# Kernel tuning notes

Measured on AMD Instinct MI355X. Metric: run time of the kernel, lower is better.

## Reference

```python
import jax, jax.numpy as jnp
import numpy as np

B, T, C, H = 4, 2048, 1024, 16


def setup_inputs() -> dict:
    key = jax.random.key(0)
    k1, k2, k3 = jax.random.split(key, 3)
    x = jax.random.normal(k1, (B, T, C), dtype=jnp.float32)
    Wqkv = jax.random.normal(k2, (C, 3 * C), dtype=jnp.float32) * 0.02
    bqkv = jnp.zeros((3 * C,), dtype=jnp.float32)
    Wproj = jax.random.normal(k3, (C, C), dtype=jnp.float32) * 0.02
    bproj = jnp.zeros((C,), dtype=jnp.float32)
    return {"x": x, "Wqkv": Wqkv, "bqkv": bqkv, "Wproj": Wproj, "bproj": bproj}


def reference(x, Wqkv, bqkv, Wproj, bproj):
    Bx, Tx, Cx = x.shape
    head = Cx // H
    qkv = x @ Wqkv + bqkv                      # [B,T,3C]
    q, k, v = jnp.split(qkv, 3, axis=-1)
    q = q.reshape(Bx, Tx, H, head)
    k = k.reshape(Bx, Tx, H, head)
    v = v.reshape(Bx, Tx, H, head)
    scale = 1.0 / jnp.sqrt(jnp.asarray(head, dtype=x.dtype))
    scores = jnp.einsum('bqhd,bkhd->bhqk', q, k) * scale   # [B,H,T,T]
    causal = jnp.tril(jnp.ones((Tx, Tx), dtype=bool))       # [T,T]
    neg = jnp.finfo(x.dtype).min
    scores = jnp.where(causal[None, None, :, :], scores, neg)
    probs = jax.nn.softmax(scores, axis=-1)
    y = jnp.einsum('bhqk,bkhd->bqhd', probs, v).reshape(Bx, Tx, Cx)
    return y @ Wproj + bproj
```

## Files before the change

### kernel.cpp

```cpp
#include <hip/hip_runtime.h>
#include <stdint.h>

#define BB 4
#define TT 2048
#define CC 1024
#define HH 16

typedef __bf16 bf16x8 __attribute__((ext_vector_type(8)));
typedef float f32x4 __attribute__((ext_vector_type(4)));
typedef float f32x16 __attribute__((ext_vector_type(16)));
typedef unsigned short ushort8 __attribute__((ext_vector_type(8)));
typedef unsigned short ushort4v __attribute__((ext_vector_type(4)));

__device__ __forceinline__ unsigned short f2b(float f) {
    union { float f; unsigned u; } v; v.f = f;
    unsigned r = v.u + 0x7FFFu + ((v.u >> 16) & 1u);
    return (unsigned short)(r >> 16);
}
__device__ __forceinline__ unsigned pack2(float a, float b) {
    union { float f; unsigned u; } ua, ub; ua.f = a; ub.f = b;
    return __builtin_amdgcn_perm(ub.u + 0x8000u, ua.u + 0x8000u, 0x07060302u);
}
__device__ __forceinline__ float fexp2(float x) {
#if __has_builtin(__builtin_amdgcn_exp2f)
    return __builtin_amdgcn_exp2f(x);
#else
    return exp2f(x);
#endif
}
#define LOG2E 1.4426950408889634f

#define ASYNC16(gp, lp) __builtin_amdgcn_global_load_lds( \
    (const __attribute__((address_space(1))) void*)(gp),  \
    (__attribute__((address_space(3))) void*)(lp), 16, 0, 0)

__global__ __launch_bounds__(256) void k_prep(const float* __restrict__ x,
                                              const float* __restrict__ Wqkv,
                                              const float* __restrict__ Wproj,
                                              unsigned short* __restrict__ x16,
                                              unsigned short* __restrict__ wqkvT,
                                              unsigned short* __restrict__ wprojT) {
    __shared__ float tile[32][33];
    const int bid = blockIdx.x;
    const int t = threadIdx.x;
    if (bid < 8192) {
        int i = (bid * 256 + t) * 4;
        float4 v = *(const float4*)(x + i);
        ushort4v o;
        o.x = f2b(v.x); o.y = f2b(v.y); o.z = f2b(v.z); o.w = f2b(v.w);
        *(ushort4v*)(x16 + i) = o;
        return;
    }
    const float* in; unsigned short* out; int R, Cc, bx, by;
    if (bid < 11264) {
        int b2 = bid - 8192;
        in = Wqkv; out = wqkvT; R = 1024; Cc = 3072;
        bx = (b2 % 96) * 32; by = (b2 / 96) * 32;
    } else {
        int b3 = bid - 11264;
        in = Wproj; out = wprojT; R = 1024; Cc = 1024;
        bx = (b3 & 31) * 32; by = (b3 >> 5) * 32;
    }
    int tx = t & 31, ty = t >> 5;
    for (int i = 0; i < 32; i += 8)
        tile[ty + i][tx] = in[(size_t)(by + ty + i) * Cc + bx + tx];
    __syncthreads();
    for (int i = 0; i < 32; i += 8)
        out[(size_t)(bx + ty + i) * R + by + tx] = f2b(tile[tx][ty + i]);
}

#define QSCALE 0.125f
template <int MODE>
__global__ __launch_bounds__(256) void k_gemm(const unsigned short* __restrict__ A,
                                              const unsigned short* __restrict__ Bt,
                                              const float* __restrict__ bias,
                                              float* __restrict__ outf,
                                              unsigned short* __restrict__ qo,
                                              unsigned short* __restrict__ ko,
                                              unsigned short* __restrict__ vo,
                                              int M, int N, int K) {
    __shared__ unsigned short sm[8704];
    unsigned short* As = sm;
    unsigned short* Bs = sm + 4096;
    const int t = threadIdx.x;
    const int lane = t & 63;
    const int c = lane & 15, qd = lane >> 4;
    const int wave = t >> 6;
    const int wr = (wave >> 1) * 64, wc = (wave & 1) * 64;
    const int bm = blockIdx.x * 128, bn = blockIdx.y * 128;

    f32x4 acc[4][4] = {};

    const unsigned short* Ap = A + (size_t)(bm + (t >> 2)) * K + (t & 3) * 8;
    const unsigned short* Bp = Bt + (size_t)(bn + (t >> 2)) * K + (t & 3) * 8;
    unsigned short* Asw = &As[t * 8];
    unsigned short* Bsw = &Bs[t * 8];

    for (int k0 = 0; k0 < K; k0 += 32) {
        __syncthreads();
        ASYNC16(Ap + k0, Asw);
        ASYNC16(Ap + (size_t)64 * K + k0, Asw + 2048);
        ASYNC16(Bp + k0, Bsw);
        ASYNC16(Bp + (size_t)64 * K + k0, Bsw + 2048);
        __syncthreads();
        bf16x8 af[4], bfr[4];
        for (int i = 0; i < 4; i++)
            af[i] = *(const bf16x8*)&As[(wr + i * 16 + c) * 32 + qd * 8];
        for (int j = 0; j < 4; j++)
            bfr[j] = *(const bf16x8*)&Bs[(wc + j * 16 + c) * 32 + qd * 8];
        for (int i = 0; i < 4; i++)
            for (int j = 0; j < 4; j++)
                acc[i][j] = __builtin_amdgcn_mfma_f32_16x16x32_bf16(af[i], bfr[j], acc[i][j], 0, 0, 0);
    }

    for (int j = 0; j < 4; j++) {
        float bv = bias[bn + wc + j * 16 + c];
        for (int i = 0; i < 4; i++)
            for (int r = 0; r < 4; r++)
                acc[i][j][r] += bv;
    }

    if (MODE == 0) {
        float* smf = (float*)sm;
        for (int p = 0; p < 4; p++) {
            __syncthreads();
            int lr0 = (wr >> 2) + qd * 4;
            for (int j = 0; j < 4; j++) {
                int col = wc + j * 16 + c;
                for (int r = 0; r < 4; r++)
                    smf[(lr0 + r) * 132 + col] = acc[p][j][r];
            }
            __syncthreads();
            for (int op = 0; op < 4; op++) {
                int lr = (t >> 5) + op * 8;
                int ch = (t & 31) * 4;
                float4 v = *(float4*)&smf[lr * 132 + ch];
                int grow = bm + (lr >> 4) * 64 + 16 * p + (lr & 15);
                *(float4*)&outf[(size_t)grow * N + bn + ch] = v;
            }
        }
    } else if (bn < 2048) {
        unsigned short* dst = (bn < 1024) ? qo : ko;
        const int dcol0 = (bn < 1024) ? bn : bn - 1024;
        const float sc = (bn < 1024) ? QSCALE : 1.0f;
        for (int p = 0; p < 2; p++) {
            __syncthreads();
            for (int ii = 0; ii < 2; ii++) {
                int i = 2 * p + ii;
                int lr0 = (wr >> 1) + ii * 16 + qd * 4;
                for (int j = 0; j < 4; j++) {
                    int col = wc + j * 16 + c;
                    for (int r = 0; r < 4; r++)
                        sm[(lr0 + r) * 136 + col] = f2b(acc[i][j][r] * sc);
                }
            }
            __syncthreads();
            for (int op = 0; op < 4; op++) {
                int lr = (t >> 4) + op * 16;
                int ch = (t & 15) * 8;
                ushort8 v = *(ushort8*)&sm[lr * 136 + ch];
                int grow = bm + (lr >> 5) * 64 + 32 * p + (lr & 31);
                *(ushort8*)&dst[(size_t)grow * 1024 + dcol0 + ch] = v;
            }
        }
    } else {
        const int bseg = bm >> 11;
        const int bmt = bm & 2047;
        for (int p = 0; p < 2; p++) {
            __syncthreads();
            for (int jj = 0; jj < 2; jj++) {
                int j = 2 * p + jj;
                int dl = (wc >> 1) + jj * 16 + c;
                for (int i = 0; i < 4; i++) {
                    int tl = wr + i * 16 + qd * 4;
                    ushort4v pk;
                    pk.x = f2b(acc[i][j][0]); pk.y = f2b(acc[i][j][1]);
                    pk.z = f2b(acc[i][j][2]); pk.w = f2b(acc[i][j][3]);
                    *(ushort4v*)&sm[dl * 136 + tl] = pk;
                }
            }
            __syncthreads();
            for (int op = 0; op < 4; op++) {
                int dl = (t >> 4) + op * 16;
                int ch = (t & 15) * 8;
                ushort8 v = *(ushort8*)&sm[dl * 136 + ch];
                int d = (bn - 2048) + (dl >> 5) * 64 + 32 * p + (dl & 31);
                *(ushort8*)&vo[((size_t)bseg * 1024 + d) * 2048 + bmt + ch] = v;
            }
        }
    }
}

__global__ __launch_bounds__(256, 4) void k_attn(const unsigned short* __restrict__ q16,
                                                 const unsigned short* __restrict__ k16,
                                                 const unsigned short* __restrict__ vT16,
                                                 unsigned short* __restrict__ y16) {
    const int h = blockIdx.y, b = blockIdx.z;
    const int qi = (((int)blockIdx.x + h) & 15) ^ ((b & 1) ? 15 : 0);
    __shared__ unsigned short smem[2 * 9216];
    unsigned short* q_s = smem;
    const int t = threadIdx.x, lane = t & 63, wave = t >> 6;
    const int l31 = lane & 31, hl = lane >> 5;
    const int wq = wave * 32;

    {
        int row = t >> 1, c32 = (t & 1) * 32;
        const unsigned short* src = q16 + ((size_t)(b * TT + qi * 128 + row)) * CC + h * 64 + c32;
        ushort8 v0 = *(const ushort8*)(src);
        ushort8 v1 = *(const ushort8*)(src + 8);
        ushort8 v2 = *(const ushort8*)(src + 16);
        ushort8 v3 = *(const ushort8*)(src + 24);
        *(ushort8*)&q_s[row * 72 + c32] = v0;
        *(ushort8*)&q_s[row * 72 + c32 + 8] = v1;
        *(ushort8*)&q_s[row * 72 + c32 + 16] = v2;
        *(ushort8*)&q_s[row * 72 + c32 + 24] = v3;
    }
    __syncthreads();
    bf16x8 qf[4];
    for (int s = 0; s < 4; s++)
        qf[s] = *(const bf16x8*)&q_s[(wq + l31) * 72 + s * 16 + hl * 8];
    __syncthreads();

    f32x16 oacc[2] = {};
    float m = -3e38f, l = 0.f;
    const int qmaxw = qi * 128 + wq + 31;
    const int qminw = qi * 128 + wq;
    const int qg = qi * 128 + wq + l31;
    const int jn = 2 * qi + 2;
    const unsigned short* kbase = k16 + (size_t)b * TT * CC + h * 64;
    const unsigned short* vbase = vT16 + (((size_t)b * 16 + h) * 64) * TT;

    const int row = t >> 2, c16 = (t & 3) * 16;
    const unsigned short* ksrc = kbase + (size_t)row * CC + c16;
    const unsigned short* vsrc = vbase + (size_t)row * TT + c16;
    ushort8 ka = *(const ushort8*)ksrc, kb = *(const ushort8*)(ksrc + 8);
    ushort8 va = *(const ushort8*)vsrc, vb = *(const ushort8*)(vsrc + 8);

    for (int j = 0; j < jn; j++) {
        unsigned short* k_s = smem + (j & 1) * 9216;
        unsigned short* vt_s = k_s + 4608;
        *(ushort8*)&k_s[row * 72 + c16] = ka;
        *(ushort8*)&k_s[row * 72 + c16 + 8] = kb;
        *(ushort8*)&vt_s[row * 72 + c16] = va;
        *(ushort8*)&vt_s[row * 72 + c16 + 8] = vb;
        __syncthreads();
        if (j + 1 < jn) {
            const unsigned short* kn = ksrc + (size_t)(j + 1) * 64 * CC;
            const unsigned short* vn = vsrc + (j + 1) * 64;
            ka = *(const ushort8*)kn; kb = *(const ushort8*)(kn + 8);
            va = *(const ushort8*)vn; vb = *(const ushort8*)(vn + 8);
        }
        if (j * 64 > qmaxw) continue;

        f32x16 sacc[2] = {};
        for (int c2 = 0; c2 < 2; c2++)
            for (int s = 0; s < 4; s++) {
                bf16x8 kf = *(const bf16x8*)&k_s[(c2 * 32 + l31) * 72 + s * 16 + hl * 8];
                sacc[c2] = __builtin_amdgcn_mfma_f32_32x32x16_bf16(kf, qf[s], sacc[c2], 0, 0, 0);
            }

        if (j * 64 + 63 > qminw) {
            for (int c2 = 0; c2 < 2; c2++)
                for (int r = 0; r < 16; r++) {
                    int kvg = j * 64 + c2 * 32 + (r & 3) + 8 * (r >> 2) + 4 * hl;
                    if (kvg > qg) sacc[c2][r] = -1e30f;
                }
        }

        float mx = -1e30f;
        for (int c2 = 0; c2 < 2; c2++)
            for (int r = 0; r < 16; r++) mx = fmaxf(mx, sacc[c2][r]);
        mx = fmaxf(mx, __shfl_xor(mx, 32, 64));
        float mn = fmaxf(m, mx);
        float negmnl = -mn * LOG2E;
        float alpha = fexp2(fmaf(m, LOG2E, negmnl));
        m = mn;
        float sum = 0.f;
        unsigned pg[2][4][2];
        for (int c2 = 0; c2 < 2; c2++)
            for (int g = 0; g < 4; g++) {
                float p0 = fexp2(fmaf(sacc[c2][g * 4 + 0], LOG2E, negmnl));
                float p1 = fexp2(fmaf(sacc[c2][g * 4 + 1], LOG2E, negmnl));
                float p2 = fexp2(fmaf(sacc[c2][g * 4 + 2], LOG2E, negmnl));
                float p3 = fexp2(fmaf(sacc[c2][g * 4 + 3], LOG2E, negmnl));
                sum += (p0 + p1) + (p2 + p3);
                pg[c2][g][0] = pack2(p0, p1);
                pg[c2][g][1] = pack2(p2, p3);
            }
        sum += __shfl_xor(sum, 32, 64);
        l = l * alpha + sum;
        if (__ballot(alpha != 1.0f)) {
            for (int c2 = 0; c2 < 2; c2++)
                for (int r = 0; r < 16; r++) oacc[c2][r] *= alpha;
        }

        bf16x8 pf[4];
        for (int c2 = 0; c2 < 2; c2++)
            for (int pr = 0; pr < 2; pr++) {
                unsigned se0 = hl ? pg[c2][2 * pr][0] : pg[c2][2 * pr + 1][0];
                unsigned se1 = hl ? pg[c2][2 * pr][1] : pg[c2][2 * pr + 1][1];
                unsigned r0 = (unsigned)__shfl_xor((int)se0, 32, 64);
                unsigned r1 = (unsigned)__shfl_xor((int)se1, 32, 64);
                union { unsigned u[4]; bf16x8 v; } fr;
                fr.u[0] = hl ? r0 : pg[c2][2 * pr][0];
                fr.u[1] = hl ? r1 : pg[c2][2 * pr][1];
                fr.u[2] = hl ? pg[c2][2 * pr + 1][0] : r0;
                fr.u[3] = hl ? pg[c2][2 * pr + 1][1] : r1;
                pf[c2 * 2 + pr] = fr.v;
            }

        for (int s = 0; s < 4; s++)
            for (int c2o = 0; c2o < 2; c2o++) {
                bf16x8 vf = *(const bf16x8*)&vt_s[(c2o * 32 + l31) * 72 + s * 16 + hl * 8];
                oacc[c2o] = __builtin_amdgcn_mfma_f32_32x32x16_bf16(vf, pf[s], oacc[c2o], 0, 0, 0);
            }
    }

    float rl = 1.0f / l;
    size_t rowb = ((size_t)b * TT + qg) * CC + h * 64;
    for (int c2 = 0; c2 < 2; c2++)
        for (int g = 0; g < 4; g++) {
            ushort4v pk;
            pk.x = f2b(oacc[c2][g * 4 + 0] * rl);
            pk.y = f2b(oacc[c2][g * 4 + 1] * rl);
            pk.z = f2b(oacc[c2][g * 4 + 2] * rl);
            pk.w = f2b(oacc[c2][g * 4 + 3] * rl);
            *(ushort4v*)&y16[rowb + c2 * 32 + g * 8 + hl * 4] = pk;
        }
}

extern "C" void kernel_launch(void* const* d_in, const int* in_sizes, int n_in,
                              void* d_out, int out_size, void* d_ws, size_t ws_size,
                              hipStream_t stream) {
    const float* x     = (const float*)d_in[0];
    const float* Wqkv  = (const float*)d_in[1];
    const float* bqkv  = (const float*)d_in[2];
    const float* Wproj = (const float*)d_in[3];
    const float* bproj = (const float*)d_in[4];
    float* out = (float*)d_out;

    const int M = BB * TT;
    unsigned short* x16    = (unsigned short*)d_ws;
    unsigned short* y16    = x16;
    unsigned short* wqkvT  = x16 + (size_t)M * CC;
    unsigned short* wprojT = wqkvT + (size_t)3 * CC * CC;
    unsigned short* q16    = wprojT + (size_t)CC * CC;
    unsigned short* k16    = q16 + (size_t)M * CC;
    unsigned short* vT16   = k16 + (size_t)M * CC;

    k_prep<<<12288, 256, 0, stream>>>(x, Wqkv, Wproj, x16, wqkvT, wprojT);
    k_gemm<1><<<dim3(M / 128, 3 * CC / 128), 256, 0, stream>>>(x16, wqkvT, bqkv, nullptr,
                                                               q16, k16, vT16, M, 3 * CC, CC);
    k_attn<<<dim3(TT / 128, HH, BB), 256, 0, stream>>>(q16, k16, vT16, y16);
    k_gemm<0><<<dim3(M / 128, CC / 128), 256, 0, stream>>>(y16, wprojT, bproj, out,
                                                           nullptr, nullptr, nullptr, M, CC, CC);
}
```

Before: 263.7 us.

## Deepen GEMM K-step to 64 and single-buffer attention K/V shared memory

The GEMM main loop now loads two 32-wide K slices per iteration into separate LDS halves, so each iteration does two MFMA passes and half as many barrier pairs run. The attention kernel drops its double-buffered K/V shared memory and reuses one 128x72 buffer, with a barrier at the top of each iteration in place of the one after the Q load. The GEMM change doubles its LDS footprint, and the attention change shrinks LDS to raise occupancy but may serialize the LDS store against the previous iteration's reads.

```diff
diff --git a/kernel.cpp b/kernel.cpp
--- a/kernel.cpp
+++ b/kernel.cpp
@@ -79,9 +79,11 @@
                                               unsigned short* __restrict__ ko,
                                               unsigned short* __restrict__ vo,
                                               int M, int N, int K) {
-    __shared__ unsigned short sm[8704];
-    unsigned short* As = sm;
-    unsigned short* Bs = sm + 4096;
+    __shared__ unsigned short sm[16384];
+    unsigned short* AsLo = sm;
+    unsigned short* AsHi = sm + 4096;
+    unsigned short* BsLo = sm + 8192;
+    unsigned short* BsHi = sm + 12288;
     const int t = threadIdx.x;
     const int lane = t & 63;
     const int c = lane & 15, qd = lane >> 4;
@@ -93,24 +95,30 @@
 
     const unsigned short* Ap = A + (size_t)(bm + (t >> 2)) * K + (t & 3) * 8;
     const unsigned short* Bp = Bt + (size_t)(bn + (t >> 2)) * K + (t & 3) * 8;
-    unsigned short* Asw = &As[t * 8];
-    unsigned short* Bsw = &Bs[t * 8];
-
-    for (int k0 = 0; k0 < K; k0 += 32) {
+
+    for (int k0 = 0; k0 < K; k0 += 64) {
         __syncthreads();
-        ASYNC16(Ap + k0, Asw);
-        ASYNC16(Ap + (size_t)64 * K + k0, Asw + 2048);
-        ASYNC16(Bp + k0, Bsw);
-        ASYNC16(Bp + (size_t)64 * K + k0, Bsw + 2048);
+        ASYNC16(Ap + k0, &AsLo[t * 8]);
+        ASYNC16(Ap + (size_t)64 * K + k0, &AsLo[t * 8 + 2048]);
+        ASYNC16(Ap + k0 + 32, &AsHi[t * 8]);
+        ASYNC16(Ap + (size_t)64 * K + k0 + 32, &AsHi[t * 8 + 2048]);
+        ASYNC16(Bp + k0, &BsLo[t * 8]);
+        ASYNC16(Bp + (size_t)64 * K + k0, &BsLo[t * 8 + 2048]);
+        ASYNC16(Bp + k0 + 32, &BsHi[t * 8]);
+        ASYNC16(Bp + (size_t)64 * K + k0 + 32, &BsHi[t * 8 + 2048]);
         __syncthreads();
-        bf16x8 af[4], bfr[4];
-        for (int i = 0; i < 4; i++)
-            af[i] = *(const bf16x8*)&As[(wr + i * 16 + c) * 32 + qd * 8];
-        for (int j = 0; j < 4; j++)
-            bfr[j] = *(const bf16x8*)&Bs[(wc + j * 16 + c) * 32 + qd * 8];
-        for (int i = 0; i < 4; i++)
+        for (int s = 0; s < 2; s++) {
+            const unsigned short* Asp = s ? AsHi : AsLo;
+            const unsigned short* Bsp = s ? BsHi : BsLo;
+            bf16x8 af[4], bfr[4];
+            for (int i = 0; i < 4; i++)
+                af[i] = *(const bf16x8*)&Asp[(wr + i * 16 + c) * 32 + qd * 8];
             for (int j = 0; j < 4; j++)
-                acc[i][j] = __builtin_amdgcn_mfma_f32_16x16x32_bf16(af[i], bfr[j], acc[i][j], 0, 0, 0);
+                bfr[j] = *(const bf16x8*)&Bsp[(wc + j * 16 + c) * 32 + qd * 8];
+            for (int i = 0; i < 4; i++)
+                for (int j = 0; j < 4; j++)
+                    acc[i][j] = __builtin_amdgcn_mfma_f32_16x16x32_bf16(af[i], bfr[j], acc[i][j], 0, 0, 0);
+        }
     }
 
     for (int j = 0; j < 4; j++) {
@@ -197,8 +205,10 @@
                                                  unsigned short* __restrict__ y16) {
     const int h = blockIdx.y, b = blockIdx.z;
     const int qi = (((int)blockIdx.x + h) & 15) ^ ((b & 1) ? 15 : 0);
-    __shared__ unsigned short smem[2 * 9216];
+    __shared__ unsigned short smem[128 * 72];
     unsigned short* q_s = smem;
+    unsigned short* k_s = smem;
+    unsigned short* vt_s = smem + 64 * 72;
     const int t = threadIdx.x, lane = t & 63, wave = t >> 6;
     const int l31 = lane & 31, hl = lane >> 5;
     const int wq = wave * 32;
@@ -219,7 +229,6 @@
     bf16x8 qf[4];
     for (int s = 0; s < 4; s++)
         qf[s] = *(const bf16x8*)&q_s[(wq + l31) * 72 + s * 16 + hl * 8];
-    __syncthreads();
 
     f32x16 oacc[2] = {};
     float m = -3e38f, l = 0.f;
@@ -237,8 +246,7 @@
     ushort8 va = *(const ushort8*)vsrc, vb = *(const ushort8*)(vsrc + 8);
 
     for (int j = 0; j < jn; j++) {
-        unsigned short* k_s = smem + (j & 1) * 9216;
-        unsigned short* vt_s = k_s + 4608;
+        __syncthreads();
         *(ushort8*)&k_s[row * 72 + c16] = ka;
         *(ushort8*)&k_s[row * 72 + c16 + 8] = kb;
         *(ushort8*)&vt_s[row * 72 + c16] = va;
```

New measurement: 271.2 us. +2.8%, slower.
